# Performance work log

Hardware: AMD Instinct MI355X
Metric: run time of the kernel (lower is better)

## Reference

```python
import jax, jax.numpy as jnp
import numpy as np

L, B, E, H, NE, K = 1024, 8, 512, 8, 8, 2
HD = E // H
SLOPE = 0.01  # LeakyReLU default negative slope
EPS = 1e-5    # LayerNorm eps


def _lin(x, w, b):
    return x @ w.T + b


def _ln(x, g, b):
    m = x.mean(-1, keepdims=True)
    v = ((x - m) ** 2).mean(-1, keepdims=True)
    return (x - m) / jnp.sqrt(v + EPS) * g + b


def _leaky(x):
    return jnp.where(x >= 0, x, SLOPE * x)


def setup_inputs() -> dict:
    key = jax.random.key(0)
    ks = jax.random.split(key, 16)
    def n(k, shape, s=0.02):
        return (jax.random.normal(k, shape) * s).astype(jnp.float32)
    z = lambda *s: jnp.zeros(s, jnp.float32)
    o = lambda *s: jnp.ones(s, jnp.float32)
    return {
        "x": jax.random.normal(ks[0], (L, B, E), jnp.float32),
        "wq": n(ks[1], (E, E)), "bq": z(E),
        "wk": n(ks[2], (E, E)), "bk": z(E),
        "wv": n(ks[3], (E, E)), "bv": z(E),
        "in_w": n(ks[4], (3 * E, E)), "in_b": z(3 * E),
        "out_w": n(ks[5], (E, E)), "out_b": z(E),
        "ln1_g": o(E), "ln1_b": z(E),
        "ln2_g": o(E), "ln2_b": z(E),
        "sh_w": n(ks[6], (E, E)), "sh_b": z(E),
        "gate_w": n(ks[7], (NE, E)), "gate_b": z(NE),
        "exp_w": n(ks[8], (NE, E, E)), "exp_b": z(NE, E),
    }


def reference(x, wq, bq, wk, bk, wv, bv, in_w, in_b, out_w, out_b,
              ln1_g, ln1_b, ln2_g, ln2_b, sh_w, sh_b,
              gate_w, gate_b, exp_w, exp_b):
    # --- outer QKV projections (to_q/to_k/to_v) ---
    q = _lin(x, wq, bq); k = _lin(x, wk, bk); v = _lin(x, wv, bv)
    # --- nn.MultiheadAttention internal in_proj + SDPA + out_proj ---
    wqi, wki, wvi = jnp.split(in_w, 3, axis=0)
    bqi, bki, bvi = jnp.split(in_b, 3)
    q = _lin(q, wqi, bqi); k = _lin(k, wki, bki); v = _lin(v, wvi, bvi)
    heads = lambda t: t.reshape(L, B, H, HD).transpose(1, 2, 0, 3)  # (B,H,L,HD)
    qh, kh, vh = heads(q), heads(k), heads(v)
    att = jax.nn.softmax(
        jnp.einsum('bhqd,bhkd->bhqk', qh, kh) / np.float32(np.sqrt(HD)), axis=-1)
    ao = jnp.einsum('bhqk,bhkd->bhqd', att, vh).transpose(2, 0, 1, 3).reshape(L, B, E)
    ao = _lin(ao, out_w, out_b)
    x1 = _ln(x + ao, ln1_g, ln1_b)
    # --- top-k MoE (vectorized dense expert eval + gather/combine) ---
    probs = jax.nn.softmax(_lin(x1, gate_w, gate_b), axis=-1)     # (L,B,NE)
    topv, topi = jax.lax.top_k(probs, K)                          # (L,B,K)
    wts = topv / topv.sum(-1, keepdims=True)
    allout = _leaky(jnp.einsum('lbe,noe->lbno', x1, exp_w) + exp_b)  # (L,B,NE,E)
    sel = jnp.take_along_axis(allout, jnp.broadcast_to(topi[..., None], (L, B, K, E)), axis=2)
    moe_out = (wts[..., None] * sel).sum(axis=2)                  # (L,B,E)
    # Switch-style load-balance auxiliary loss
    mask = jax.nn.one_hot(topi, NE, dtype=x1.dtype).sum(axis=2)   # (L,B,NE)
    f = mask.reshape(-1, NE).mean(0)
    P = probs.reshape(-1, NE).mean(0)
    gating_loss = NE * jnp.sum(f * P)
    # --- shared expert + residual + LN ---
    shared = _leaky(_lin(x1, sh_w, sh_b))
    x2 = _ln(x1 + moe_out + shared, ln2_g, ln2_b)
    return (x2, gating_loss)
```

## Files before the change

kernel.cpp:

```cpp
#include <hip/hip_runtime.h>
#include <stdint.h>

#define LL   1024
#define BB   8
#define EE   512
#define HH   8
#define HDD  64
#define NEXP 8
#define TT   8192

typedef unsigned short u16t;
typedef __bf16 bf16x8 __attribute__((ext_vector_type(8)));
typedef u16t   u16x8  __attribute__((ext_vector_type(8)));
typedef u16t   u16x4  __attribute__((ext_vector_type(4)));
typedef float  f32x4  __attribute__((ext_vector_type(4)));

#define LAM 0.18033688011112042f

__device__ __forceinline__ u16t f2bf(float f) {
  union { float f; unsigned int u; } a; a.f = f;
  unsigned int r = a.u + 0x7fffu + ((a.u >> 16) & 1u);
  return (u16t)(r >> 16);
}
__device__ __forceinline__ float bf2f(u16t s) {
  union { unsigned int u; float f; } a; a.u = ((unsigned int)s) << 16; return a.f;
}

__device__ __forceinline__ f32x4 mfma16(bf16x8 a, bf16x8 b, f32x4 c) {
  return __builtin_amdgcn_mfma_f32_16x16x32_bf16(a, b, c, 0, 0, 0);
}

#define GLDS16(gp, lp) \
  __builtin_amdgcn_global_load_lds( \
      (const __attribute__((address_space(1))) unsigned int*)(const void*)(gp), \
      (__attribute__((address_space(3))) unsigned int*)(void*)(lp), 16, 0, 0)

__global__ __launch_bounds__(256) void cvt_all(
    const float* __restrict__ x, const float* __restrict__ in_w,
    const float* __restrict__ out_w, const float* __restrict__ shw,
    const float* __restrict__ expw,
    const float* __restrict__ wq, const float* __restrict__ wk,
    const float* __restrict__ wv,
    u16t* __restrict__ xb, u16t* __restrict__ inwb, u16t* __restrict__ outwb,
    u16t* __restrict__ shwb, u16t* __restrict__ expwb, u16t* __restrict__ w3t) {
  __shared__ float tile[64][65];
  const int bid = blockIdx.x;
  if (bid >= 7424) {
    const int i = bid - 7424;
    const int z = i >> 6, rem = i & 63;
    const int by = rem >> 3, bx = rem & 7;
    const float* src = z == 0 ? wq : z == 1 ? wk : wv;
    u16t* dst = w3t + (size_t)z * 262144;
    const int r = threadIdx.x >> 4;
    const int c = (threadIdx.x & 15) * 4;
    const int r0 = by * 64, c0 = bx * 64;
#pragma unroll
    for (int k = 0; k < 4; k++) {
      float4 v = *(const float4*)&src[(size_t)(r0 + r + k * 16) * 512 + c0 + c];
      tile[r + k * 16][c] = v.x; tile[r + k * 16][c + 1] = v.y;
      tile[r + k * 16][c + 2] = v.z; tile[r + k * 16][c + 3] = v.w;
    }
    __syncthreads();
#pragma unroll
    for (int k = 0; k < 4; k++) {
      const int orow = c0 + r + k * 16;
      u16x4 o = { f2bf(tile[c][r + k * 16]), f2bf(tile[c + 1][r + k * 16]),
                  f2bf(tile[c + 2][r + k * 16]), f2bf(tile[c + 3][r + k * 16]) };
      *(u16x4*)&dst[(size_t)orow * 512 + r0 + c] = o;
    }
    return;
  }
  const float* s; u16t* d; int i;
  if (bid < 4096)      { s = x;     d = xb;    i = bid; }
  else if (bid < 4864) { s = in_w;  d = inwb;  i = bid - 4096; }
  else if (bid < 5120) { s = out_w; d = outwb; i = bid - 4864; }
  else if (bid < 5376) { s = shw;   d = shwb;  i = bid - 5120; }
  else                 { s = expw;  d = expwb; i = bid - 5376; }
  const int idx = (i * 256 + threadIdx.x) * 4;
  float4 v = *(const float4*)&s[idx];
  u16x4 o = { f2bf(v.x), f2bf(v.y), f2bf(v.z), f2bf(v.w) };
  *(u16x4*)&d[idx] = o;
}

__global__ __launch_bounds__(256) void compose_k(const u16t* __restrict__ Aall,
                                                 const u16t* __restrict__ Wall,
                                                 u16t* __restrict__ Call) {
  const u16t* A = Aall + (size_t)blockIdx.z * 262144;
  const u16t* W = Wall + (size_t)blockIdx.z * 262144;
  u16t* C = Call + (size_t)blockIdx.z * 262144;
  const float scale = blockIdx.z == 0 ? LAM : 1.0f;
  __shared__ alignas(16) u16t As[64 * 32];
  __shared__ alignas(16) u16t Ws[64 * 32];
  const int tid = threadIdx.x;
  const int lane = tid & 63, wave = tid >> 6;
  const int r15 = lane & 15, rhi = lane >> 4;
  const int wr = wave >> 1, wc = wave & 1;
  const int m0 = blockIdx.x * 64, n0 = blockIdx.y * 64;
  const int arow = tid >> 2, acol = (tid & 3) * 8;
  const f32x4 fz = {0.f, 0.f, 0.f, 0.f};
  f32x4 acc[2][2] = {{fz, fz}, {fz, fz}};
  const u16t* Ap = A + (size_t)(m0 + arow) * 512 + acol;
  const u16t* Wp = W + (size_t)(n0 + arow) * 512 + acol;
  u16t* As0 = &As[tid * 8];
  u16t* Ws0 = &Ws[tid * 8];
  for (int kt = 0; kt < 512; kt += 32) {
    __syncthreads();
    GLDS16(Ap + kt, As0);
    GLDS16(Wp + kt, Ws0);
    asm volatile("s_waitcnt vmcnt(0)" ::: "memory");
    __syncthreads();
    bf16x8 af[2], bfv[2];
#pragma unroll
    for (int mi = 0; mi < 2; mi++)
      af[mi] = *(const bf16x8*)&As[(wr * 32 + mi * 16 + r15) * 32 + rhi * 8];
#pragma unroll
    for (int ni = 0; ni < 2; ni++)
      bfv[ni] = *(const bf16x8*)&Ws[(wc * 32 + ni * 16 + r15) * 32 + rhi * 8];
#pragma unroll
    for (int mi = 0; mi < 2; mi++)
#pragma unroll
      for (int ni = 0; ni < 2; ni++)
        acc[mi][ni] = mfma16(af[mi], bfv[ni], acc[mi][ni]);
  }
#pragma unroll
  for (int mi = 0; mi < 2; mi++)
#pragma unroll
    for (int ni = 0; ni < 2; ni++) {
      const int col = n0 + wc * 32 + ni * 16 + r15;
#pragma unroll
      for (int r = 0; r < 4; r++) {
        const int row = m0 + wr * 32 + mi * 16 + rhi * 4 + r;
        C[(size_t)row * 512 + col] = f2bf(acc[mi][ni][r] * scale);
      }
    }
}

__global__ __launch_bounds__(256) void bias_mv(const float* __restrict__ in_w,
                                               const float* __restrict__ in_b,
                                               const float* __restrict__ b0,
                                               const float* __restrict__ b1,
                                               const float* __restrict__ b2v,
                                               float* __restrict__ out) {
  const int bi = blockIdx.x;
  const int seg = bi >> 3, m0 = (bi & 7) * 64;
  const float* bvec = seg == 0 ? b0 : seg == 1 ? b1 : b2v;
  const int m = m0 + (threadIdx.x >> 2), q = threadIdx.x & 3;
  const float* row = in_w + (size_t)(seg * 512 + m) * 512 + q * 128;
  const float* bv = bvec + q * 128;
  float s = 0.f;
  for (int j = 0; j < 128; j++) s += row[j] * bv[j];
  s += __shfl_xor(s, 1); s += __shfl_xor(s, 2);
  if (q == 0) {
    float r2 = s + in_b[seg * 512 + m];
    out[seg * 512 + m] = seg == 0 ? r2 * LAM : r2;
  }
}

template<int ACT, int OUTBF>
__global__ __launch_bounds__(256) void gemm_bt(
    const u16t* __restrict__ A, int lda,
    const u16t* __restrict__ W,
    const float* __restrict__ bias,
    void* __restrict__ Cp, int ldc, int K)
{
  __shared__ alignas(16) u16t As[2 * 128 * 32];
  __shared__ alignas(16) u16t Ws[2 * 128 * 32];
  const int tid  = threadIdx.x;
  const int lane = tid & 63, wave = tid >> 6;
  const int r15  = lane & 15, rhi = lane >> 4;
  const int wr   = wave >> 1, wc  = wave & 1;
  const int m0 = blockIdx.x * 128, n0 = blockIdx.y * 128;
  const int arow = tid >> 2, acol = (tid & 3) * 8;

  const f32x4 fz = {0.f, 0.f, 0.f, 0.f};
  f32x4 acc[4][4];
#pragma unroll
  for (int i = 0; i < 4; i++)
#pragma unroll
    for (int j = 0; j < 4; j++) acc[i][j] = fz;

  const u16t* Ap0 = A + (size_t)(m0 + arow) * lda + acol;
  const u16t* Ap1 = A + (size_t)(m0 + arow + 64) * lda + acol;
  const u16t* Wp0 = W + (size_t)(n0 + arow) * K + acol;
  const u16t* Wp1 = W + (size_t)(n0 + arow + 64) * K + acol;

  GLDS16(Ap0, &As[tid * 8]);
  GLDS16(Ap1, &As[(tid + 256) * 8]);
  GLDS16(Wp0, &Ws[tid * 8]);
  GLDS16(Wp1, &Ws[(tid + 256) * 8]);

  int cur = 0;
  for (int kt = 0; kt < K; kt += 32) {
    const int nxt = cur ^ 1;
    if (kt) __syncthreads();
    if (kt + 32 < K) {
      const int no = nxt * 4096;
      GLDS16(Ap0 + kt + 32, &As[no + tid * 8]);
      GLDS16(Ap1 + kt + 32, &As[no + (tid + 256) * 8]);
      GLDS16(Wp0 + kt + 32, &Ws[no + tid * 8]);
      GLDS16(Wp1 + kt + 32, &Ws[no + (tid + 256) * 8]);
      asm volatile("s_waitcnt vmcnt(4)" ::: "memory");
    } else {
      asm volatile("s_waitcnt vmcnt(0)" ::: "memory");
    }
    __syncthreads();
    const int cb = cur * 4096;
    bf16x8 af[4], bfv[4];
#pragma unroll
    for (int mi = 0; mi < 4; mi++)
      af[mi] = *(const bf16x8*)&As[cb + (wr * 64 + mi * 16 + r15) * 32 + rhi * 8];
#pragma unroll
    for (int ni = 0; ni < 4; ni++)
      bfv[ni] = *(const bf16x8*)&Ws[cb + (wc * 64 + ni * 16 + r15) * 32 + rhi * 8];
#pragma unroll
    for (int mi = 0; mi < 4; mi++)
#pragma unroll
      for (int ni = 0; ni < 4; ni++)
        acc[mi][ni] = mfma16(af[mi], bfv[ni], acc[mi][ni]);
    cur = nxt;
  }

#pragma unroll
  for (int mi = 0; mi < 4; mi++) {
#pragma unroll
    for (int ni = 0; ni < 4; ni++) {
      const int col = n0 + wc * 64 + ni * 16 + r15;
      const float bv = bias[col];
#pragma unroll
      for (int r = 0; r < 4; r++) {
        const int row = m0 + wr * 64 + mi * 16 + rhi * 4 + r;
        float v = acc[mi][ni][r] + bv;
        if (ACT == 1) v = v >= 0.f ? v : 0.01f * v;
        if (OUTBF) ((u16t*)Cp)[(size_t)row * ldc + col] = f2bf(v);
        else       ((float*)Cp)[(size_t)row * ldc + col] = v;
      }
    }
  }
}

template<int ACT>
__global__ __launch_bounds__(256) void gemm64(
    const u16t* __restrict__ A, int lda,
    const u16t* __restrict__ W,
    const float* __restrict__ bias,
    u16t* __restrict__ Cp, int ldc, int K)
{
  __shared__ alignas(16) u16t As[2 * 64 * 32];
  __shared__ alignas(16) u16t Ws[2 * 64 * 32];
  const int tid  = threadIdx.x;
  const int lane = tid & 63, wave = tid >> 6;
  const int r15  = lane & 15, rhi = lane >> 4;
  const int wr   = wave >> 1, wc  = wave & 1;
  const int m0 = blockIdx.x * 64, n0 = blockIdx.y * 64;
  const int arow = tid >> 2, acol = (tid & 3) * 8;

  const f32x4 fz = {0.f, 0.f, 0.f, 0.f};
  f32x4 acc[2][2] = {{fz, fz}, {fz, fz}};

  const u16t* Ap = A + (size_t)(m0 + arow) * lda + acol;
  const u16t* Wp = W + (size_t)(n0 + arow) * K + acol;

  GLDS16(Ap, &As[tid * 8]);
  GLDS16(Wp, &Ws[tid * 8]);

  int cur = 0;
  for (int kt = 0; kt < K; kt += 32) {
    const int nxt = cur ^ 1;
    if (kt) __syncthreads();
    if (kt + 32 < K) {
      const int no = nxt * 2048;
      GLDS16(Ap + kt + 32, &As[no + tid * 8]);
      GLDS16(Wp + kt + 32, &Ws[no + tid * 8]);
      asm volatile("s_waitcnt vmcnt(2)" ::: "memory");
    } else {
      asm volatile("s_waitcnt vmcnt(0)" ::: "memory");
    }
    __syncthreads();
    const int cb = cur * 2048;
    bf16x8 af[2], bfv[2];
#pragma unroll
    for (int mi = 0; mi < 2; mi++)
      af[mi] = *(const bf16x8*)&As[cb + (wr * 32 + mi * 16 + r15) * 32 + rhi * 8];
#pragma unroll
    for (int ni = 0; ni < 2; ni++)
      bfv[ni] = *(const bf16x8*)&Ws[cb + (wc * 32 + ni * 16 + r15) * 32 + rhi * 8];
#pragma unroll
    for (int mi = 0; mi < 2; mi++)
#pragma unroll
      for (int ni = 0; ni < 2; ni++)
        acc[mi][ni] = mfma16(af[mi], bfv[ni], acc[mi][ni]);
    cur = nxt;
  }

#pragma unroll
  for (int mi = 0; mi < 2; mi++)
#pragma unroll
    for (int ni = 0; ni < 2; ni++) {
      const int col = n0 + wc * 32 + ni * 16 + r15;
      const float bv = bias[col];
#pragma unroll
      for (int r = 0; r < 4; r++) {
        const int row = m0 + wr * 32 + mi * 16 + rhi * 4 + r;
        float v = acc[mi][ni][r] + bv;
        if (ACT == 1) v = v >= 0.f ? v : 0.01f * v;
        Cp[(size_t)row * ldc + col] = f2bf(v);
      }
    }
}

#define MOE_MAX_TILES 200
__global__ __launch_bounds__(256) void moe_shared(
    const u16t* __restrict__ x1b, const u16t* __restrict__ expwb,
    const float* __restrict__ expb,
    const u16t* __restrict__ shwb, const float* __restrict__ shb,
    const int* __restrict__ counts,
    const int* __restrict__ list, const float* __restrict__ wlist,
    u16t* __restrict__ out_slots, u16t* __restrict__ shrd)
{
  const int raw = blockIdx.x;
  const int idx = (raw & 7) * 25 + (raw >> 3);
  int e = 0, base = 0, cnt = 0;
  for (; e < 8; e++) {
    cnt = counts[e];
    const int nt = (cnt + 127) >> 7;
    if (idx < base + nt) break;
    base += nt;
  }
  const bool sh = (e == 8);
  if (sh) {
    cnt = TT;
    if (idx - base >= 64) return;
  }
  const int m0 = (idx - base) * 128;
  if (m0 >= cnt) return;

  const int n0 = blockIdx.y * 128;
  __shared__ alignas(16) u16t As[2 * 128 * 32];
  __shared__ alignas(16) u16t Ws[2 * 128 * 32];
  __shared__ int tks[128];
  __shared__ float wws[128];
  const int tid  = threadIdx.x;
  const int lane = tid & 63, wave = tid >> 6;
  const int r15  = lane & 15, rhi = lane >> 4;
  const int wr   = wave >> 1, wc  = wave & 1;
  const int arow = tid >> 2, acol = (tid & 3) * 8;

  if (tid < 128) {
    if (sh) { tks[tid] = m0 + tid; wws[tid] = 1.f; }
    else {
      int i2 = m0 + tid; if (i2 >= cnt) i2 = cnt - 1;
      tks[tid] = list[e * 8192 + i2];
      wws[tid] = wlist[e * 8192 + i2];
    }
  }
  __syncthreads();
  const int tokA = sh ? tks[arow] : (tks[arow] >> 1);
  const int tokB = sh ? tks[arow + 64] : (tks[arow + 64] >> 1);

  const f32x4 fz = {0.f, 0.f, 0.f, 0.f};
  f32x4 acc[4][4];
#pragma unroll
  for (int i = 0; i < 4; i++)
#pragma unroll
    for (int j = 0; j < 4; j++) acc[i][j] = fz;

  const u16t* Ap0 = x1b + (size_t)tokA * 512 + acol;
  const u16t* Ap1 = x1b + (size_t)tokB * 512 + acol;
  const u16t* W  = (sh ? shwb : expwb + (size_t)e * 262144);
  const float* bias = sh ? shb : expb + e * 512;
  u16t* outp = sh ? shrd : out_slots;
  const u16t* Wp0 = W + (size_t)(n0 + arow) * 512 + acol;
  const u16t* Wp1 = Wp0 + (size_t)64 * 512;

  GLDS16(Ap0, &As[tid * 8]);
  GLDS16(Ap1, &As[(tid + 256) * 8]);
  GLDS16(Wp0, &Ws[tid * 8]);
  GLDS16(Wp1, &Ws[(tid + 256) * 8]);

  int cur = 0;
  for (int kt = 0; kt < 512; kt += 32) {
    const int nxt = cur ^ 1;
    if (kt) __syncthreads();
    if (kt + 32 < 512) {
      const int no = nxt * 4096;
      GLDS16(Ap0 + kt + 32, &As[no + tid * 8]);
      GLDS16(Ap1 + kt + 32, &As[no + (tid + 256) * 8]);
      GLDS16(Wp0 + kt + 32, &Ws[no + tid * 8]);
      GLDS16(Wp1 + kt + 32, &Ws[no + (tid + 256) * 8]);
      asm volatile("s_waitcnt vmcnt(4)" ::: "memory");
    } else {
      asm volatile("s_waitcnt vmcnt(0)" ::: "memory");
    }
    __syncthreads();
    const int cb = cur * 4096;
    bf16x8 af[4], bfv[4];
#pragma unroll
    for (int mi = 0; mi < 4; mi++)
      af[mi] = *(const bf16x8*)&As[cb + (wr * 64 + mi * 16 + r15) * 32 + rhi * 8];
#pragma unroll
    for (int ni = 0; ni < 4; ni++)
      bfv[ni] = *(const bf16x8*)&Ws[cb + (wc * 64 + ni * 16 + r15) * 32 + rhi * 8];
#pragma unroll
    for (int mi = 0; mi < 4; mi++)
#pragma unroll
      for (int ni = 0; ni < 4; ni++)
        acc[mi][ni] = mfma16(af[mi], bfv[ni], acc[mi][ni]);
    cur = nxt;
  }

#pragma unroll
  for (int mi = 0; mi < 4; mi++)
#pragma unroll
    for (int ni = 0; ni < 4; ni++) {
      const int col = n0 + wc * 64 + ni * 16 + r15;
      const float bv = bias[col];
#pragma unroll
      for (int r = 0; r < 4; r++) {
        const int rl = wr * 64 + mi * 16 + rhi * 4 + r;
        if (m0 + rl < cnt) {
          float z = acc[mi][ni][r] + bv;
          z = z >= 0.f ? z : 0.01f * z;
          outp[(size_t)tks[rl] * 512 + col] = f2bf(wws[rl] * z);
        }
      }
    }
}

__global__ __launch_bounds__(512) void attn_kernel(
    const u16t* __restrict__ qkv, u16t* __restrict__ ao)
{
  const int bh = blockIdx.x;
  const int b = bh >> 3, h = bh & 7;
  const int qg = blockIdx.y;
  const int tid  = threadIdx.x;
  const int lane = tid & 63, wave = tid >> 6;
  const int r15  = lane & 15, rhi = lane >> 4;

  __shared__ alignas(16) u16t Ks[128 * 72];
  __shared__ alignas(16) u16t Vt[64 * 136];

  const int qrow = qg * 128 + (wave >> 2) * 64 + (wave & 3) * 16 + r15;
  const size_t qoff = ((size_t)qrow * BB + b) * 1536 + h * HDD;
  const bf16x8 qf0 = *(const bf16x8*)&qkv[qoff + rhi * 8];
  const bf16x8 qf1 = *(const bf16x8*)&qkv[qoff + 32 + rhi * 8];

  const f32x4 fz = {0.f, 0.f, 0.f, 0.f};
  f32x4 oa[4] = {fz, fz, fz, fz};
  float psum = 0.f;

  const int krow = tid >> 2, kchunk = (tid & 3) * 16;
  const int vd0 = (wave & 3) * 16 + (lane >> 5) * 8;
  const int vkv = (wave >> 2) * 64 + (lane & 31) * 2;

  u16x8 kA0, kA1, vA0, vA1;
  {
    const size_t kb = ((size_t)krow * BB + b) * 1536 + h * HDD + 512 + kchunk;
    kA0 = *(const u16x8*)&qkv[kb];
    kA1 = *(const u16x8*)&qkv[kb + 8];
    const size_t v0 = ((size_t)vkv * BB + b) * 1536 + h * HDD + 1024 + vd0;
    vA0 = *(const u16x8*)&qkv[v0];
    vA1 = *(const u16x8*)&qkv[v0 + (size_t)BB * 1536];
  }

  for (int t = 0; t < 8; t++) {
    __syncthreads();
    {
      u16t* kd = &Ks[krow * 72 + kchunk];
      *(u16x8*)&kd[0] = kA0;
      *(u16x8*)&kd[8] = kA1;
    }
#pragma unroll
    for (int j = 0; j < 8; j++) {
      unsigned int w = (unsigned int)vA0[j] | ((unsigned int)vA1[j] << 16);
      *(unsigned int*)&Vt[(vd0 + j) * 136 + vkv] = w;
    }
    if (t < 7) {
      const int kv0n = (t + 1) * 128;
      const size_t kb = ((size_t)(kv0n + krow) * BB + b) * 1536 + h * HDD + 512 + kchunk;
      kA0 = *(const u16x8*)&qkv[kb];
      kA1 = *(const u16x8*)&qkv[kb + 8];
      const size_t v0 = ((size_t)(kv0n + vkv) * BB + b) * 1536 + h * HDD + 1024 + vd0;
      vA0 = *(const u16x8*)&qkv[v0];
      vA1 = *(const u16x8*)&qkv[v0 + (size_t)BB * 1536];
    }
    __syncthreads();

    f32x4 s[8];
    __builtin_amdgcn_s_setprio(1);
#pragma unroll
    for (int nt = 0; nt < 8; nt++) {
      const u16t* kr = &Ks[(nt * 16 + r15) * 72];
      bf16x8 k0 = *(const bf16x8*)&kr[rhi * 8];
      bf16x8 k1 = *(const bf16x8*)&kr[32 + rhi * 8];
      f32x4 acc = fz;
      acc = mfma16(k0, qf0, acc);
      acc = mfma16(k1, qf1, acc);
      s[nt] = acc;
    }
    __builtin_amdgcn_s_setprio(0);

    unsigned int P2[8][2];
#pragma unroll
    for (int nt = 0; nt < 8; nt++) {
#pragma unroll
      for (int r = 0; r < 4; r++) {
        s[nt][r] = exp2f(s[nt][r]);
        psum += s[nt][r];
      }
      asm("v_cvt_pk_bf16_f32 %0, %1, %2" : "=v"(P2[nt][0]) : "v"(s[nt][0]), "v"(s[nt][1]));
      asm("v_cvt_pk_bf16_f32 %0, %1, %2" : "=v"(P2[nt][1]) : "v"(s[nt][2]), "v"(s[nt][3]));
    }

    __builtin_amdgcn_s_setprio(1);
#pragma unroll
    for (int c = 0; c < 4; c++) {
      union { unsigned int w[4]; bf16x8 v; } pf;
      pf.w[0] = P2[2 * c][0];     pf.w[1] = P2[2 * c][1];
      pf.w[2] = P2[2 * c + 1][0]; pf.w[3] = P2[2 * c + 1][1];
#pragma unroll
      for (int dd = 0; dd < 4; dd++) {
        const u16t* vr = &Vt[(dd * 16 + r15) * 136 + c * 32 + rhi * 4];
        union { u16x4 h[2]; bf16x8 v; } vb;
        vb.h[0] = *(const u16x4*)&vr[0];
        vb.h[1] = *(const u16x4*)&vr[16];
        oa[dd] = mfma16(vb.v, pf.v, oa[dd]);
      }
    }
    __builtin_amdgcn_s_setprio(0);
  }

  float ls = psum;
  ls += __shfl_xor(ls, 16);
  ls += __shfl_xor(ls, 32);
  const float inv = 1.f / ls;
  const size_t obase = ((size_t)qrow * BB + b) * EE + h * HDD;
#pragma unroll
  for (int dd = 0; dd < 4; dd++) {
    u16x4 o = { f2bf(oa[dd][0] * inv), f2bf(oa[dd][1] * inv),
                f2bf(oa[dd][2] * inv), f2bf(oa[dd][3] * inv) };
    *(u16x4*)&ao[obase + dd * 16 + rhi * 4] = o;
  }
}

__device__ __forceinline__ float wave_sum(float v) {
#pragma unroll
  for (int off = 1; off < 64; off <<= 1) v += __shfl_xor(v, off);
  return v;
}

__global__ __launch_bounds__(256) void ln1_gate(
    const float* __restrict__ x, const u16t* __restrict__ aopb,
    const float* __restrict__ g, const float* __restrict__ be,
    const float* __restrict__ gw, const float* __restrict__ gb,
    u16t* __restrict__ x1b,
    int* __restrict__ tok_pack, float2* __restrict__ tok_w,
    float* __restrict__ partials)
{
  const int wave = threadIdx.x >> 6, lane = threadIdx.x & 63;
  const int t = blockIdx.x * 4 + wave;
  const size_t base = (size_t)t * EE + lane * 8;
  float4 a0 = *(const float4*)&x[base], a1 = *(const float4*)&x[base + 4];
  u16x8 ap = *(const u16x8*)&aopb[base];
  float v[8] = { a0.x + bf2f(ap[0]), a0.y + bf2f(ap[1]), a0.z + bf2f(ap[2]), a0.w + bf2f(ap[3]),
                 a1.x + bf2f(ap[4]), a1.y + bf2f(ap[5]), a1.z + bf2f(ap[6]), a1.w + bf2f(ap[7]) };
  float s = 0.f;
#pragma unroll
  for (int i = 0; i < 8; i++) s += v[i];
  const float mean = wave_sum(s) * (1.f / EE);
  float vs = 0.f;
#pragma unroll
  for (int i = 0; i < 8; i++) { v[i] -= mean; vs += v[i] * v[i]; }
  const float inv = rsqrtf(wave_sum(vs) * (1.f / EE) + 1e-5f);
  float4 g0 = *(const float4*)&g[lane * 8],  g1 = *(const float4*)&g[lane * 8 + 4];
  float4 b0 = *(const float4*)&be[lane * 8], b1 = *(const float4*)&be[lane * 8 + 4];
  float o[8] = { v[0]*inv*g0.x + b0.x, v[1]*inv*g0.y + b0.y, v[2]*inv*g0.z + b0.z, v[3]*inv*g0.w + b0.w,
                 v[4]*inv*g1.x + b1.x, v[5]*inv*g1.y + b1.y, v[6]*inv*g1.z + b1.z, v[7]*inv*g1.w + b1.w };
  u16x8 ob = { f2bf(o[0]), f2bf(o[1]), f2bf(o[2]), f2bf(o[3]),
               f2bf(o[4]), f2bf(o[5]), f2bf(o[6]), f2bf(o[7]) };
  *(u16x8*)&x1b[base] = ob;

  float pe[8];
  float mx = -1e30f;
#pragma unroll
  for (int e = 0; e < 8; e++) {
    float4 ga = *(const float4*)&gw[e * EE + lane * 8];
    float4 gB = *(const float4*)&gw[e * EE + lane * 8 + 4];
    float d = o[0]*ga.x + o[1]*ga.y + o[2]*ga.z + o[3]*ga.w
            + o[4]*gB.x + o[5]*gB.y + o[6]*gB.z + o[7]*gB.w;
#pragma unroll
    for (int off = 1; off < 64; off <<= 1) d += __shfl_xor(d, off);
    pe[e] = d + gb[e];
    mx = fmaxf(mx, pe[e]);
  }
  float se = 0.f;
#pragma unroll
  for (int e = 0; e < 8; e++) { pe[e] = __expf(pe[e] - mx); se += pe[e]; }
  const float invs = 1.f / se;
#pragma unroll
  for (int e = 0; e < 8; e++) pe[e] *= invs;
  float v1 = -1.f; int i1 = 0;
#pragma unroll
  for (int e = 0; e < 8; e++) if (pe[e] > v1) { v1 = pe[e]; i1 = e; }
  float v2 = -1.f; int i2 = -1;
#pragma unroll
  for (int e = 0; e < 8; e++) if (e != i1 && pe[e] > v2) { v2 = pe[e]; i2 = e; }
  const float denom = 1.f / (v1 + v2);
  if (lane == 0) {
    tok_pack[t] = i1 | (i2 << 8);
    float2 w; w.x = v1 * denom; w.y = v2 * denom;
    tok_w[t] = w;
  }
  __shared__ float fb[4][8], pb[4][8];
  if (lane < 8) {
    fb[wave][lane] = (lane == i1 || lane == i2) ? 1.f : 0.f;
    pb[wave][lane] = pe[lane];
  }
  __syncthreads();
  if (threadIdx.x < 8) {
    const int e = threadIdx.x;
    partials[(size_t)blockIdx.x * 16 + e]     = fb[0][e] + fb[1][e] + fb[2][e] + fb[3][e];
    partials[(size_t)blockIdx.x * 16 + 8 + e] = pb[0][e] + pb[1][e] + pb[2][e] + pb[3][e];
  }
}

__global__ __launch_bounds__(256) void ln2_kernel(
    const u16t* __restrict__ x1b, const u16t* __restrict__ slots,
    const u16t* __restrict__ sh,
    const float* __restrict__ g, const float* __restrict__ be,
    float* __restrict__ out)
{
  const int wave = threadIdx.x >> 6, lane = threadIdx.x & 63;
  const int t = blockIdx.x * 4 + wave;
  const size_t base = (size_t)t * EE + lane * 8;
  u16x8 xv = *(const u16x8*)&x1b[base];
  u16x8 m0 = *(const u16x8*)&slots[(size_t)(2 * t) * EE + lane * 8];
  u16x8 m1 = *(const u16x8*)&slots[(size_t)(2 * t + 1) * EE + lane * 8];
  u16x8 sv = *(const u16x8*)&sh[base];
  float v[8];
#pragma unroll
  for (int i = 0; i < 8; i++)
    v[i] = bf2f(xv[i]) + bf2f(m0[i]) + bf2f(m1[i]) + bf2f(sv[i]);
  float s = 0.f;
#pragma unroll
  for (int i = 0; i < 8; i++) s += v[i];
  const float mean = wave_sum(s) * (1.f / EE);
  float vs = 0.f;
#pragma unroll
  for (int i = 0; i < 8; i++) { v[i] -= mean; vs += v[i] * v[i]; }
  const float inv = rsqrtf(wave_sum(vs) * (1.f / EE) + 1e-5f);
  float4 g0 = *(const float4*)&g[lane * 8],  g1 = *(const float4*)&g[lane * 8 + 4];
  float4 b0 = *(const float4*)&be[lane * 8], b1 = *(const float4*)&be[lane * 8 + 4];
  *(float4*)&out[base] = make_float4(v[0]*inv*g0.x + b0.x, v[1]*inv*g0.y + b0.y,
                                     v[2]*inv*g0.z + b0.z, v[3]*inv*g0.w + b0.w);
  *(float4*)&out[base + 4] = make_float4(v[4]*inv*g1.x + b1.x, v[5]*inv*g1.y + b1.y,
                                         v[6]*inv*g1.z + b1.z, v[7]*inv*g1.w + b1.w);
}

__global__ __launch_bounds__(512) void build_lists(
    const int* __restrict__ tok_pack, const float2* __restrict__ tok_w,
    int* __restrict__ counts, int* __restrict__ list, float* __restrict__ wlist,
    const float* __restrict__ partials, float* __restrict__ loss_out)
{
  if (blockIdx.x == 8) {
    __shared__ float acc2[32][16];
    __shared__ float fin[16];
    const int c = threadIdx.x & 15, grp = threadIdx.x >> 4;
    float s = 0.f;
    for (int i = grp; i < 2048; i += 32) s += partials[(size_t)i * 16 + c];
    acc2[grp][c] = s;
    __syncthreads();
    if (threadIdx.x < 16) {
      float t2 = 0.f;
      for (int g2 = 0; g2 < 32; g2++) t2 += acc2[g2][threadIdx.x];
      fin[threadIdx.x] = t2;
    }
    __syncthreads();
    if (threadIdx.x == 0) {
      float loss = 0.f;
      for (int e = 0; e < 8; e++)
        loss += (fin[e] * (1.f / TT)) * (fin[8 + e] * (1.f / TT));
      loss_out[0] = loss * 8.f;
    }
    return;
  }
  const int e = blockIdx.x;
  const int tid = threadIdx.x;
  const int lane = tid & 63, wave = tid >> 6;
  __shared__ int wtot[8];
  __shared__ int runb;
  if (tid == 0) runb = 0;
  __syncthreads();
  for (int c = 0; c < 16; c++) {
    const int t = c * 512 + tid;
    const int pk = tok_pack[t];
    const int i1 = pk & 255, i2 = (pk >> 8) & 255;
    const bool s1 = (i1 == e);
    const bool flag = s1 || (i2 == e);
    const unsigned long long mask = __ballot(flag);
    if (lane == 63) wtot[wave] = __popcll(mask);
    __syncthreads();
    int wbase = 0;
#pragma unroll
    for (int w2 = 0; w2 < 8; w2++) if (w2 < wave) wbase += wtot[w2];
    int btot = 0;
#pragma unroll
    for (int w2 = 0; w2 < 8; w2++) btot += wtot[w2];
    if (flag) {
      const int pre = __popcll(mask & ((1ull << lane) - 1ull));
      const int pos = runb + wbase + pre;
      list[e * 8192 + pos] = 2 * t + (s1 ? 0 : 1);
      float2 w = tok_w[t];
      wlist[e * 8192 + pos] = s1 ? w.x : w.y;
    }
    __syncthreads();
    if (tid == 0) runb += btot;
    __syncthreads();
  }
  if (tid == 0) counts[e] = runb;
}

extern "C" void kernel_launch(void* const* d_in, const int* in_sizes, int n_in,
                              void* d_out, int out_size, void* d_ws, size_t ws_size,
                              hipStream_t stream) {
  const float* x    = (const float*)d_in[0];
  const float* wq   = (const float*)d_in[1];
  const float* bq   = (const float*)d_in[2];
  const float* wk   = (const float*)d_in[3];
  const float* bk   = (const float*)d_in[4];
  const float* wv   = (const float*)d_in[5];
  const float* bv   = (const float*)d_in[6];
  const float* in_w = (const float*)d_in[7];
  const float* in_b = (const float*)d_in[8];
  const float* out_w= (const float*)d_in[9];
  const float* out_b= (const float*)d_in[10];
  const float* ln1g = (const float*)d_in[11];
  const float* ln1b = (const float*)d_in[12];
  const float* ln2g = (const float*)d_in[13];
  const float* ln2b = (const float*)d_in[14];
  const float* shw  = (const float*)d_in[15];
  const float* shb  = (const float*)d_in[16];
  const float* gw   = (const float*)d_in[17];
  const float* gb   = (const float*)d_in[18];
  const float* expw = (const float*)d_in[19];
  const float* expb = (const float*)d_in[20];

  char* ws = (char*)d_ws;
  u16t* xb     = (u16t*)(ws + 0);
  u16t* inwb   = (u16t*)(ws + 8388608);
  u16t* w3t    = (u16t*)(ws + 9961472);
  u16t* w2big  = (u16t*)(ws + 11534336);
  u16t* outwb  = (u16t*)(ws + 13107200);
  u16t* shwb   = (u16t*)(ws + 13631488);
  u16t* expwb  = (u16t*)(ws + 14155776);
  float* b2    = (float*)(ws + 18350080);
  int*  tok_pack = (int*)(ws + 18356224);
  float2* tok_w  = (float2*)(ws + 18388992);
  int*  counts = (int*)(ws + 18454528);
  int*  list   = (int*)(ws + 18454656);
  float* wlist = (float*)(ws + 18716800);
  float* parts = (float*)(ws + 18978944);
  const size_t S = 19110016;
  u16t* qkvb   = (u16t*)(ws + S);
  u16t* aopb   = (u16t*)(ws + S);
  u16t* x1b    = (u16t*)(ws + S + 16777216);
  u16t* oslots = (u16t*)(ws + S);
  u16t* aob    = (u16t*)(ws + 0);
  u16t* shrd   = (u16t*)(ws + 0);
  float* outp  = (float*)d_out;

  dim3 blk(256);
  cvt_all<<<7616, blk, 0, stream>>>(x, in_w, out_w, shw, expw, wq, wk, wv,
                                    xb, inwb, outwb, shwb, expwb, w3t);
  compose_k<<<dim3(8, 8, 3), blk, 0, stream>>>(inwb, w3t, w2big);
  bias_mv<<<24, blk, 0, stream>>>(in_w, in_b, bq, bk, bv, b2);
  gemm_bt<0,1><<<dim3(64, 12), blk, 0, stream>>>(xb, EE, w2big, b2, qkvb, 1536, EE);
  attn_kernel<<<dim3(64, 8), dim3(512), 0, stream>>>(qkvb, aob);
  gemm64<0><<<dim3(128, 8), blk, 0, stream>>>(aob, EE, outwb, out_b, aopb, EE, EE);
  ln1_gate<<<2048, blk, 0, stream>>>(x, aopb, ln1g, ln1b, gw, gb, x1b, tok_pack, tok_w, parts);
  build_lists<<<9, dim3(512), 0, stream>>>(tok_pack, tok_w, counts, list, wlist,
                                           parts, outp + (size_t)TT * EE);
  moe_shared<<<dim3(MOE_MAX_TILES, 4), blk, 0, stream>>>(x1b, expwb, expb, shwb, shb,
                                                         counts, list, wlist, oslots, shrd);
  ln2_kernel<<<2048, blk, 0, stream>>>(x1b, oslots, shrd, ln2g, ln2b, outp);
}
```

Before: 171.7 us.

## Pre-gather expert inputs into contiguous rows and scatter via slot positions in LN2

Adds a gather kernel that copies each expert's routed token rows of x1 into a contiguous buffer, so the MoE GEMM reads and writes contiguous rows instead of doing indexed per-row loads and scattered stores. build_lists now records a slot-to-position map, and ln2 uses it together with prefix sums of the counts to fetch each token's two expert outputs. This removes the indirect addressing from the GEMM's A loads and its epilogue stores. In exchange it adds a kernel launch and an extra round trip of about 16K rows through memory.

```diff
diff --git a/kernel.cpp b/kernel.cpp
--- a/kernel.cpp
+++ b/kernel.cpp
@@ -308,23 +308,46 @@
     }
 }
 
+__global__ __launch_bounds__(256) void gather_x(
+    const u16t* __restrict__ x1b, const int* __restrict__ list,
+    const int* __restrict__ counts, u16t* __restrict__ xg)
+{
+  const int e = blockIdx.x, c = blockIdx.y;
+  const int cnt = counts[e];
+  const int pos0 = c * 128;
+  if (pos0 >= cnt) return;
+  int rowbase = 0;
+  for (int j = 0; j < e; j++) rowbase += counts[j];
+  const int chunk = threadIdx.x & 63;
+  const int rsub = threadIdx.x >> 6;
+  for (int p = 0; p < 32; p++) {
+    const int pos = pos0 + p * 4 + rsub;
+    if (pos < cnt) {
+      const int tok = list[e * 8192 + pos] >> 1;
+      *(u16x8*)&xg[(size_t)(rowbase + pos) * 512 + chunk * 8] =
+          *(const u16x8*)&x1b[(size_t)tok * 512 + chunk * 8];
+    }
+  }
+}
+
 #define MOE_MAX_TILES 200
 __global__ __launch_bounds__(256) void moe_shared(
-    const u16t* __restrict__ x1b, const u16t* __restrict__ expwb,
+    const u16t* __restrict__ xg, const u16t* __restrict__ expwb,
     const float* __restrict__ expb,
+    const u16t* __restrict__ x1b,
     const u16t* __restrict__ shwb, const float* __restrict__ shb,
-    const int* __restrict__ counts,
-    const int* __restrict__ list, const float* __restrict__ wlist,
-    u16t* __restrict__ out_slots, u16t* __restrict__ shrd)
+    const int* __restrict__ counts, const float* __restrict__ wlist,
+    u16t* __restrict__ yg, u16t* __restrict__ shrd)
 {
   const int raw = blockIdx.x;
   const int idx = (raw & 7) * 25 + (raw >> 3);
-  int e = 0, base = 0, cnt = 0;
+  int e = 0, base = 0, cnt = 0, rowbase = 0;
   for (; e < 8; e++) {
     cnt = counts[e];
     const int nt = (cnt + 127) >> 7;
     if (idx < base + nt) break;
     base += nt;
+    rowbase += cnt;
   }
   const bool sh = (e == 8);
   if (sh) {
@@ -337,7 +360,6 @@
   const int n0 = blockIdx.y * 128;
   __shared__ alignas(16) u16t As[2 * 128 * 32];
   __shared__ alignas(16) u16t Ws[2 * 128 * 32];
-  __shared__ int tks[128];
   __shared__ float wws[128];
   const int tid  = threadIdx.x;
   const int lane = tid & 63, wave = tid >> 6;
@@ -346,16 +368,13 @@
   const int arow = tid >> 2, acol = (tid & 3) * 8;
 
   if (tid < 128) {
-    if (sh) { tks[tid] = m0 + tid; wws[tid] = 1.f; }
+    if (sh) wws[tid] = 1.f;
     else {
       int i2 = m0 + tid; if (i2 >= cnt) i2 = cnt - 1;
-      tks[tid] = list[e * 8192 + i2];
       wws[tid] = wlist[e * 8192 + i2];
     }
   }
   __syncthreads();
-  const int tokA = sh ? tks[arow] : (tks[arow] >> 1);
-  const int tokB = sh ? tks[arow + 64] : (tks[arow + 64] >> 1);
 
   const f32x4 fz = {0.f, 0.f, 0.f, 0.f};
   f32x4 acc[4][4];
@@ -364,11 +383,18 @@
 #pragma unroll
     for (int j = 0; j < 4; j++) acc[i][j] = fz;
 
-  const u16t* Ap0 = x1b + (size_t)tokA * 512 + acol;
-  const u16t* Ap1 = x1b + (size_t)tokB * 512 + acol;
+  const u16t *Ap0, *Ap1;
+  if (sh) {
+    Ap0 = x1b + (size_t)(m0 + arow) * 512 + acol;
+    Ap1 = Ap0 + (size_t)64 * 512;
+  } else {
+    int rA = rowbase + m0 + arow;      if (rA > 16383) rA = 16383;
+    int rB = rowbase + m0 + arow + 64; if (rB > 16383) rB = 16383;
+    Ap0 = xg + (size_t)rA * 512 + acol;
+    Ap1 = xg + (size_t)rB * 512 + acol;
+  }
   const u16t* W  = (sh ? shwb : expwb + (size_t)e * 262144);
   const float* bias = sh ? shb : expb + e * 512;
-  u16t* outp = sh ? shrd : out_slots;
   const u16t* Wp0 = W + (size_t)(n0 + arow) * 512 + acol;
   const u16t* Wp1 = Wp0 + (size_t)64 * 512;
 
@@ -408,6 +434,8 @@
     cur = nxt;
   }
 
+  u16t* Obase = sh ? (shrd + (size_t)m0 * 512)
+                   : (yg + (size_t)(rowbase + m0) * 512);
 #pragma unroll
   for (int mi = 0; mi < 4; mi++)
 #pragma unroll
@@ -420,7 +448,7 @@
         if (m0 + rl < cnt) {
           float z = acc[mi][ni][r] + bv;
           z = z >= 0.f ? z : 0.01f * z;
-          outp[(size_t)tks[rl] * 512 + col] = f2bf(wws[rl] * z);
+          Obase[(size_t)rl * 512 + col] = f2bf(wws[rl] * z);
         }
       }
     }
@@ -624,17 +652,28 @@
 }
 
 __global__ __launch_bounds__(256) void ln2_kernel(
-    const u16t* __restrict__ x1b, const u16t* __restrict__ slots,
+    const u16t* __restrict__ x1b, const u16t* __restrict__ yg,
+    const int* __restrict__ slotpos, const int* __restrict__ counts,
     const u16t* __restrict__ sh,
     const float* __restrict__ g, const float* __restrict__ be,
     float* __restrict__ out)
 {
+  __shared__ int pf[8];
+  if (threadIdx.x < 8) {
+    int s2 = 0;
+    for (int j = 0; j < (int)threadIdx.x; j++) s2 += counts[j];
+    pf[threadIdx.x] = s2;
+  }
+  __syncthreads();
   const int wave = threadIdx.x >> 6, lane = threadIdx.x & 63;
   const int t = blockIdx.x * 4 + wave;
   const size_t base = (size_t)t * EE + lane * 8;
+  const int v0p = slotpos[2 * t], v1p = slotpos[2 * t + 1];
+  const int row0 = pf[v0p >> 13] + (v0p & 8191);
+  const int row1 = pf[v1p >> 13] + (v1p & 8191);
   u16x8 xv = *(const u16x8*)&x1b[base];
-  u16x8 m0 = *(const u16x8*)&slots[(size_t)(2 * t) * EE + lane * 8];
-  u16x8 m1 = *(const u16x8*)&slots[(size_t)(2 * t + 1) * EE + lane * 8];
+  u16x8 m0 = *(const u16x8*)&yg[(size_t)row0 * EE + lane * 8];
+  u16x8 m1 = *(const u16x8*)&yg[(size_t)row1 * EE + lane * 8];
   u16x8 sv = *(const u16x8*)&sh[base];
   float v[8];
 #pragma unroll
@@ -659,6 +698,7 @@
 __global__ __launch_bounds__(512) void build_lists(
     const int* __restrict__ tok_pack, const float2* __restrict__ tok_w,
     int* __restrict__ counts, int* __restrict__ list, float* __restrict__ wlist,
+    int* __restrict__ slotpos,
     const float* __restrict__ partials, float* __restrict__ loss_out)
 {
   if (blockIdx.x == 8) {
@@ -708,7 +748,9 @@
     if (flag) {
       const int pre = __popcll(mask & ((1ull << lane) - 1ull));
       const int pos = runb + wbase + pre;
-      list[e * 8192 + pos] = 2 * t + (s1 ? 0 : 1);
+      const int slot = 2 * t + (s1 ? 0 : 1);
+      list[e * 8192 + pos] = slot;
+      slotpos[slot] = e * 8192 + pos;
       float2 w = tok_w[t];
       wlist[e * 8192 + pos] = s1 ? w.x : w.y;
     }
@@ -759,13 +801,15 @@
   int*  list   = (int*)(ws + 18454656);
   float* wlist = (float*)(ws + 18716800);
   float* parts = (float*)(ws + 18978944);
-  const size_t S = 19110016;
+  int* slotpos = (int*)(ws + 19107072);
+  const size_t S = 19173120;
   u16t* qkvb   = (u16t*)(ws + S);
   u16t* aopb   = (u16t*)(ws + S);
   u16t* x1b    = (u16t*)(ws + S + 16777216);
-  u16t* oslots = (u16t*)(ws + S);
+  u16t* yg     = (u16t*)(ws + S);
   u16t* aob    = (u16t*)(ws + 0);
   u16t* shrd   = (u16t*)(ws + 0);
+  u16t* xg     = (u16t*)(ws + S + 25165824);
   float* outp  = (float*)d_out;
 
   dim3 blk(256);
@@ -778,8 +822,9 @@
   gemm64<0><<<dim3(128, 8), blk, 0, stream>>>(aob, EE, outwb, out_b, aopb, EE, EE);
   ln1_gate<<<2048, blk, 0, stream>>>(x, aopb, ln1g, ln1b, gw, gb, x1b, tok_pack, tok_w, parts);
   build_lists<<<9, dim3(512), 0, stream>>>(tok_pack, tok_w, counts, list, wlist,
-                                           parts, outp + (size_t)TT * EE);
-  moe_shared<<<dim3(MOE_MAX_TILES, 4), blk, 0, stream>>>(x1b, expwb, expb, shwb, shb,
-                                                         counts, list, wlist, oslots, shrd);
-  ln2_kernel<<<2048, blk, 0, stream>>>(x1b, oslots, shrd, ln2g, ln2b, outp);
-}
+                                           slotpos, parts, outp + (size_t)TT * EE);
+  gather_x<<<dim3(8, 64), blk, 0, stream>>>(x1b, list, counts, xg);
+  moe_shared<<<dim3(MOE_MAX_TILES, 4), blk, 0, stream>>>(xg, expwb, expb, x1b, shwb, shb,
+                                                         counts, wlist, yg, shrd);
+  ln2_kernel<<<2048, blk, 0, stream>>>(x1b, yg, slotpos, counts, shrd, ln2g, ln2b, outp);
+}
```

Result: slower. 192.5 us (+12.1%).
